# Kernel optimization log

Measured on AMD Instinct MI355X. Metric: run time of the kernel, lower is better.

The kernel has to match this reference:

```python
import jax, jax.numpy as jnp
import numpy as np

N, D, K_FRAC = 4096, 256, 0.5
EPS = 1e-5  # BatchNorm1d default eps


def setup_inputs() -> dict:
    key = jax.random.key(0)
    kg, kh, kw = jax.random.split(key, 3)
    # sparse binary adjacency with self-loops so all degrees > 0 (pow(D,-1) finite)
    g = (jax.random.uniform(kg, (N, N)) < 0.004).astype(jnp.float32)
    g = jnp.maximum(g, jnp.eye(N, dtype=jnp.float32))
    h = jax.random.normal(kh, (N, D), dtype=jnp.float32)
    return {
        "g": g,
        "h": h,
        "gamma": jnp.ones((D,), jnp.float32),
        "beta": jnp.zeros((D,), jnp.float32),
        "w_proj": jax.random.normal(kw, (D, 1), dtype=jnp.float32) / np.sqrt(D),
        "b_proj": jnp.zeros((1,), jnp.float32),
        "sigma1": jnp.array([0.2], jnp.float32),
    }


def reference(g, h, gamma, beta, w_proj, b_proj, sigma1):
    # BatchNorm1d in training mode: batch statistics over the node axis
    mu = h.mean(0)
    var = h.var(0)  # biased variance, as torch uses for normalization
    h = (h - mu) / jnp.sqrt(var + EPS) * gamma + beta

    deg = g.sum(1)                               # [N] == Z2
    agg = (g @ h) / deg[:, None]                 # diag(D^-1) @ (g @ h), no NxN diag materialized
    Z1 = jnp.abs(h - agg).sum(1)                 # [N]
    pl = jax.nn.sigmoid(Z1 + deg)
    Z3 = (agg @ w_proj + b_proj)[:, 0]           # proj(Z3).squeeze()
    pg = jax.nn.softmax(Z3)                      # 1-D softmax (dim 0)
    pt = jax.nn.sigmoid(pl + pg)
    pf = jax.nn.sigmoid((h @ w_proj + b_proj)[:, 0])
    scores = sigma1[0] * pt + (1.0 - sigma1[0]) * pf

    # top_k_graph
    k = max(2, int(K_FRAC * N))
    _, idx = jax.lax.top_k(scores, k)            # [k]
    h_att = scores[:, None] * h                  # score-weighted features
    un_g = (g != 0).astype(jnp.float32)
    two_hop = ((un_g @ un_g) != 0).astype(jnp.float32)  # binarized 2-hop adjacency
    a_hat = two_hop[idx, :]                      # [k, N] row gather
    new_h = a_hat @ h_att                        # [k, D]
    g_new = a_hat[:, idx]                        # [k, k] column gather
    # norm_g: torch broadcast divides COLUMN j by row-sum degrees[j]
    g_new = g_new / g_new.sum(1)
    return g_new, new_h, idx
```

## Files before the change

### kernel.cpp

```cpp
#include <hip/hip_runtime.h>
#include <math.h>

#define NN 4096
#define DD 256
#define KK 2048
#define NW 64
#define SK 4
#define KC (NN / SK)
#define KW (KC / 32)

typedef float f32x4  __attribute__((ext_vector_type(4)));
typedef short bf16x8 __attribute__((ext_vector_type(8)));

__device__ __forceinline__ int build_list(const unsigned long long* __restrict__ B, int r,
                                          int l, int* cols, int cap) {
    unsigned long long word = B[(size_t)r * NW + l];
    int pc = __popcll(word);
    int off = pc;
    for (int d = 1; d < 64; d <<= 1) {
        int n = __shfl_up(off, d);
        if (l >= d) off += n;
    }
    int total = __shfl(off, 63);
    int base = off - pc;
    while (word) {
        int b = (int)__ffsll(word) - 1;
        word &= word - 1;
        if (base < cap) cols[base] = l * 64 + b;
        ++base;
    }
    return total;
}

__global__ void k_pre(const float* __restrict__ h, const float* __restrict__ g,
                      double* __restrict__ psum, double* __restrict__ psq,
                      unsigned long long* __restrict__ B) {
    int blk = blockIdx.x;
    int t = threadIdx.x;
    if (blk < 64) {
        int d = t;
        int r0 = blk * 64;
        double s0=0,s1=0,s2=0,s3=0,q0=0,q1=0,q2=0,q3=0;
        for (int k = 0; k < 64; k += 4) {
            double x0 = (double)h[(size_t)(r0+k+0) * DD + d];
            double x1 = (double)h[(size_t)(r0+k+1) * DD + d];
            double x2 = (double)h[(size_t)(r0+k+2) * DD + d];
            double x3 = (double)h[(size_t)(r0+k+3) * DD + d];
            s0 += x0; q0 += x0*x0;
            s1 += x1; q1 += x1*x1;
            s2 += x2; q2 += x2*x2;
            s3 += x3; q3 += x3*x3;
        }
        psum[blk * DD + d] = (s0+s1)+(s2+s3);
        psq [blk * DD + d] = (q0+q1)+(q2+q3);
    } else {
        int i = blk - 64;
        int q = t >> 6, l = t & 63;
        const float* gr = g + (size_t)i * NN;
        unsigned long long word = 0ull;
        int lw = l & 15;
        #pragma unroll
        for (int wi = 0; wi < 16; ++wi) {
            float v = gr[(q * 16 + wi) * 64 + l];
            unsigned long long m = __ballot(v != 0.0f);
            if (wi == lw) word = m;
        }
        if (l < 16) B[(size_t)i * NW + q * 16 + l] = word;
    }
}

__global__ void k_stats_final(const double* __restrict__ psum, const double* __restrict__ psq,
                              double* __restrict__ mu, double* __restrict__ rstd) {
    __shared__ double rs[4][DD];
    __shared__ double rq[4][DD];
    int t = threadIdx.x;
    int d = t & (DD - 1);
    int q = t >> 8;
    double s0=0,s1=0,q0=0,q1=0;
    int b0 = q * 16;
    for (int k = 0; k < 16; k += 2) {
        s0 += psum[(b0+k)   * DD + d];
        s1 += psum[(b0+k+1) * DD + d];
        q0 += psq [(b0+k)   * DD + d];
        q1 += psq [(b0+k+1) * DD + d];
    }
    rs[q][d] = s0 + s1;
    rq[q][d] = q0 + q1;
    __syncthreads();
    if (q == 0) {
        double S  = (rs[0][d]+rs[1][d]) + (rs[2][d]+rs[3][d]);
        double Q  = (rq[0][d]+rq[1][d]) + (rq[2][d]+rq[3][d]);
        double m  = S / (double)NN;
        double var = Q / (double)NN - m * m;
        mu[d]   = m;
        rstd[d] = 1.0 / sqrt(var + 1e-5);
    }
}

__global__ void k_main(const float* __restrict__ h, const double* __restrict__ mu,
                       const double* __restrict__ rstd, const float* __restrict__ gamma,
                       const float* __restrict__ beta, const unsigned long long* __restrict__ Bm,
                       const float* __restrict__ w, const float* __restrict__ bp,
                       float* __restrict__ hn, double* __restrict__ zpf,
                       unsigned long long* __restrict__ T, double* __restrict__ Z1,
                       double* __restrict__ Z3, int* __restrict__ degi) {
    __shared__ int cols[4][136];
    int blk = blockIdx.x;
    int t = threadIdx.x;
    int wv = t >> 6, l = t & 63;
    int r = blk * 4 + wv;
    int cnt = build_list(Bm, r, l, cols[wv], 128);
    if (cnt > 128) cnt = 128;
    const float4* h4 = (const float4*)h;
    double s0=0,s1=0,s2=0,s3=0,u0=0,u1=0,u2=0,u3=0;
    unsigned long long a0 = 0ull, a1 = 0ull;
    int j = 0;
    for (; j + 1 < cnt; j += 2) {
        int c0 = cols[wv][j], c1 = cols[wv][j + 1];
        float4 v0 = h4[(size_t)c0 * 64 + l];
        float4 v1 = h4[(size_t)c1 * 64 + l];
        a0 |= Bm[(size_t)c0 * NW + l];
        a1 |= Bm[(size_t)c1 * NW + l];
        s0 += (double)v0.x; s1 += (double)v0.y; s2 += (double)v0.z; s3 += (double)v0.w;
        u0 += (double)v1.x; u1 += (double)v1.y; u2 += (double)v1.z; u3 += (double)v1.w;
    }
    if (j < cnt) {
        int c0 = cols[wv][j];
        float4 v0 = h4[(size_t)c0 * 64 + l];
        a0 |= Bm[(size_t)c0 * NW + l];
        s0 += (double)v0.x; s1 += (double)v0.y; s2 += (double)v0.z; s3 += (double)v0.w;
    }
    T[(size_t)r * NW + l] = a0 | a1;
    s0 += u0; s1 += u1; s2 += u2; s3 += u3;
    const double2* mu2 = (const double2*)mu;
    const double2* rs2 = (const double2*)rstd;
    const float4*  ga4 = (const float4*)gamma;
    const float4*  be4 = (const float4*)beta;
    const float4*  w4  = (const float4*)w;
    double2 mA = mu2[2*l], mB = mu2[2*l+1];
    double2 rA = rs2[2*l], rB = rs2[2*l+1];
    float4 ga = ga4[l], be = be4[l], wl = w4[l];
    double inv = 1.0 / (double)cnt;
    double g0 = (s0 * inv - mA.x) * rA.x * (double)ga.x + (double)be.x;
    double g1 = (s1 * inv - mA.y) * rA.y * (double)ga.y + (double)be.y;
    double g2 = (s2 * inv - mB.x) * rB.x * (double)ga.z + (double)be.z;
    double g3 = (s3 * inv - mB.y) * rB.y * (double)ga.w + (double)be.w;
    float4 hv = h4[(size_t)r * 64 + l];
    double h0 = ((double)hv.x - mA.x) * rA.x * (double)ga.x + (double)be.x;
    double h1 = ((double)hv.y - mA.y) * rA.y * (double)ga.y + (double)be.y;
    double h2 = ((double)hv.z - mB.x) * rB.x * (double)ga.z + (double)be.z;
    double h3 = ((double)hv.w - mB.y) * rB.y * (double)ga.w + (double)be.w;
    float4 o = { (float)h0, (float)h1, (float)h2, (float)h3 };
    ((float4*)hn)[(size_t)r * 64 + l] = o;
    double z1p = (fabs(h0 - g0) + fabs(h1 - g1)) + (fabs(h2 - g2) + fabs(h3 - g3));
    double z3p = (g0 * (double)wl.x + g1 * (double)wl.y)
               + (g2 * (double)wl.z + g3 * (double)wl.w);
    double zfp = (h0 * (double)wl.x + h1 * (double)wl.y)
               + (h2 * (double)wl.z + h3 * (double)wl.w);
    for (int off = 32; off > 0; off >>= 1) {
        z1p += __shfl_down(z1p, off);
        z3p += __shfl_down(z3p, off);
        zfp += __shfl_down(zfp, off);
    }
    if (l == 0) {
        Z1[r] = z1p;
        Z3[r] = z3p + (double)bp[0];
        zpf[r] = zfp + (double)bp[0];
        degi[r] = cnt;
    }
}

__global__ void k_sel(const double* __restrict__ Z1, const double* __restrict__ Z3,
                      const double* __restrict__ zpf, const int* __restrict__ degi,
                      const float* __restrict__ sigma1, const float* __restrict__ hn,
                      unsigned short* __restrict__ haT_hi, unsigned short* __restrict__ haT_lo,
                      int* __restrict__ idx_int, float* __restrict__ out_idx) {
    __shared__ unsigned long long Kl[NN];
    double* red = (double*)Kl;
    int bid = blockIdx.x;
    int t = threadIdx.x;
    int wv = t >> 6, l = t & 63;
    double mx = -1e300;
    for (int k = 0; k < 16; ++k) mx = fmax(mx, Z3[t + 256 * k]);
    red[t] = mx;
    __syncthreads();
    for (int s = 128; s > 0; s >>= 1) {
        if (t < s) red[t] = fmax(red[t], red[t + s]);
        __syncthreads();
    }
    double M = red[0];
    __syncthreads();
    double se = 0.0;
    for (int k = 0; k < 16; ++k) se += exp(Z3[t + 256 * k] - M);
    red[t] = se;
    __syncthreads();
    for (int s = 128; s > 0; s >>= 1) {
        if (t < s) red[t] += red[t + s];
        __syncthreads();
    }
    double sum = red[0];
    double s1 = (double)sigma1[0];
    __syncthreads();
    if (bid < 256) {
        for (int i = t; i < NN; i += 256) {
            double pg = exp(Z3[i] - M) / sum;
            double pl = 1.0 / (1.0 + exp(-(Z1[i] + (double)degi[i])));
            double pt = 1.0 / (1.0 + exp(-(pl + pg)));
            double pf = 1.0 / (1.0 + exp(-zpf[i]));
            float sc = (float)(s1 * pt + (1.0 - s1) * pf);
            unsigned int b2 = __float_as_uint(sc);
            unsigned int ka = (b2 & 0x80000000u) ? ~b2 : (b2 ^ 0x80000000u);
            Kl[i] = ((unsigned long long)(~ka) << 32) | (unsigned int)i;
        }
        __syncthreads();
        int il = t >> 4, sub = t & 15;
        int i = bid * 16 + il;
        unsigned long long ki = Kl[i];
        int c0 = 0, c1 = 0, c2 = 0, c3 = 0;
        for (int jj = 0; jj < 256; jj += 4) {
            int jx = sub + (jj << 4);
            c0 += (Kl[jx]      < ki) ? 1 : 0;
            c1 += (Kl[jx + 16] < ki) ? 1 : 0;
            c2 += (Kl[jx + 32] < ki) ? 1 : 0;
            c3 += (Kl[jx + 48] < ki) ? 1 : 0;
        }
        int cnt = (c0 + c1) + (c2 + c3);
        for (int off = 8; off > 0; off >>= 1) cnt += __shfl_down(cnt, off, 16);
        if (sub == 0 && cnt < KK) {
            idx_int[cnt] = i;
            out_idx[cnt] = (float)i;
        }
    } else {
        int bb = bid - 256;
        int ng = bb & 63, dq = bb >> 6;
        int node = ng * 64 + l;
        double pg = exp(Z3[node] - M) / sum;
        double pl = 1.0 / (1.0 + exp(-(Z1[node] + (double)degi[node])));
        double pt = 1.0 / (1.0 + exp(-(pl + pg)));
        double pf = 1.0 / (1.0 + exp(-zpf[node]));
        float sc = (float)(s1 * pt + (1.0 - s1) * pf);
        const float* hr = hn + (size_t)node * DD;
        for (int d = dq * 64 + wv; d < (dq + 1) * 64; d += 4) {
            float x = hr[d] * sc;
            unsigned int xb = __float_as_uint(x);
            unsigned int hb = xb & 0xFFFF0000u;
            float lo = x - __uint_as_float(hb);
            unsigned int lb = __float_as_uint(lo);
            haT_hi[(size_t)d * NN + node] = (unsigned short)(hb >> 16);
            haT_lo[(size_t)d * NN + node] = (unsigned short)(lb >> 16);
        }
    }
}

__global__ void k_out(const unsigned long long* __restrict__ T, const int* __restrict__ idx_int,
                      const unsigned short* __restrict__ haT_hi,
                      const unsigned short* __restrict__ haT_lo,
                      float* __restrict__ part, float* __restrict__ out_gnew) {
    union Sm {
        struct { unsigned long long Tl[NW]; int redc[4]; } og;
        struct { int ids[128]; unsigned int Ab[128][KW + 1]; } nh;
    };
    __shared__ Sm sm;
    int bid = blockIdx.x;
    int t = threadIdx.x;
    int wv = t >> 6, l = t & 63;
    if (bid < 256) {
        int blk = bid;
        int rs = blk & 15, cb = (blk >> 4) & 3, kc = blk >> 6;
        if (t < 128) sm.nh.ids[t] = idx_int[rs * 128 + t];
        __syncthreads();
        for (int i = t; i < 128 * KW; i += 256) {
            int row = i >> 5, wd = i & (KW - 1);
            sm.nh.Ab[row][wd] =
                ((const unsigned int*)(T + (size_t)sm.nh.ids[row] * NW))[kc * KW + wd];
        }
        __syncthreads();
        int lm = l & 15, lg = l >> 4;
        int row_base = (wv & 1) * 64;
        int col_base = cb * 64 + (wv >> 1) * 32;
        f32x4 acc[4][2];
        #pragma unroll
        for (int m = 0; m < 4; ++m) { acc[m][0] = (f32x4)0.0f; acc[m][1] = (f32x4)0.0f; }
        const unsigned short* ph0 = haT_hi + (size_t)(col_base + lm) * NN + kc * KC + lg * 8;
        const unsigned short* ph1 = ph0 + (size_t)16 * NN;
        const unsigned short* pl0 = haT_lo + (size_t)(col_base + lm) * NN + kc * KC + lg * 8;
        const unsigned short* pl1 = pl0 + (size_t)16 * NN;
        #pragma unroll 2
        for (int ks = 0; ks < KW; ++ks) {
            bf16x8 bh0 = *(const bf16x8*)(ph0 + ks * 32);
            bf16x8 bh1 = *(const bf16x8*)(ph1 + ks * 32);
            bf16x8 bl0 = *(const bf16x8*)(pl0 + ks * 32);
            bf16x8 bl1 = *(const bf16x8*)(pl1 + ks * 32);
            #pragma unroll
            for (int m = 0; m < 4; ++m) {
                unsigned int bits = sm.nh.Ab[row_base + m * 16 + lm][ks];
                unsigned int b8 = (bits >> (8 * lg)) & 0xFFu;
                union { unsigned int u[4]; bf16x8 v; } au;
                au.u[0] = ((b8 & 1u)        ? 0x3F80u : 0u) | ((b8 & 2u)   ? 0x3F800000u : 0u);
                au.u[1] = (((b8 >> 2) & 1u) ? 0x3F80u : 0u) | ((b8 & 8u)   ? 0x3F800000u : 0u);
                au.u[2] = (((b8 >> 4) & 1u) ? 0x3F80u : 0u) | ((b8 & 32u)  ? 0x3F800000u : 0u);
                au.u[3] = (((b8 >> 6) & 1u) ? 0x3F80u : 0u) | ((b8 & 128u) ? 0x3F800000u : 0u);
                bf16x8 a = au.v;
                acc[m][0] = __builtin_amdgcn_mfma_f32_16x16x32_bf16(a, bh0, acc[m][0], 0, 0, 0);
                acc[m][1] = __builtin_amdgcn_mfma_f32_16x16x32_bf16(a, bh1, acc[m][1], 0, 0, 0);
                acc[m][0] = __builtin_amdgcn_mfma_f32_16x16x32_bf16(a, bl0, acc[m][0], 0, 0, 0);
                acc[m][1] = __builtin_amdgcn_mfma_f32_16x16x32_bf16(a, bl1, acc[m][1], 0, 0, 0);
            }
        }
        float* pp = part + (size_t)kc * ((size_t)KK * DD);
        #pragma unroll
        for (int m = 0; m < 4; ++m) {
            int row0 = rs * 128 + row_base + m * 16 + lg * 4;
            #pragma unroll
            for (int n = 0; n < 2; ++n) {
                int col = col_base + n * 16 + lm;
                #pragma unroll
                for (int rr = 0; rr < 4; ++rr)
                    pp[(size_t)(row0 + rr) * DD + col] = acc[m][n][rr];
            }
        }
    } else {
        int r = bid - 256;
        if (t < NW) sm.og.Tl[t] = T[(size_t)idx_int[r] * NW + t];
        __syncthreads();
        const int4* idx4 = (const int4*)idx_int;
        int cloc = 0;
        for (int c4 = t; c4 < KK / 4; c4 += 256) {
            int4 jc = idx4[c4];
            cloc += (int)((sm.og.Tl[jc.x >> 6] >> (jc.x & 63)) & 1ull)
                  + (int)((sm.og.Tl[jc.y >> 6] >> (jc.y & 63)) & 1ull)
                  + (int)((sm.og.Tl[jc.z >> 6] >> (jc.z & 63)) & 1ull)
                  + (int)((sm.og.Tl[jc.w >> 6] >> (jc.w & 63)) & 1ull);
        }
        for (int off = 32; off > 0; off >>= 1) cloc += __shfl_down(cloc, off);
        if (l == 0) sm.og.redc[wv] = cloc;
        __syncthreads();
        float inv = 1.0f / (float)((sm.og.redc[0] + sm.og.redc[1])
                                 + (sm.og.redc[2] + sm.og.redc[3]));
        float4* out4 = (float4*)(out_gnew + (size_t)r * KK);
        for (int c4 = t; c4 < KK / 4; c4 += 256) {
            int4 jc = idx4[c4];
            float4 o;
            o.x = ((sm.og.Tl[jc.x >> 6] >> (jc.x & 63)) & 1ull) ? inv : 0.0f;
            o.y = ((sm.og.Tl[jc.y >> 6] >> (jc.y & 63)) & 1ull) ? inv : 0.0f;
            o.z = ((sm.og.Tl[jc.z >> 6] >> (jc.z & 63)) & 1ull) ? inv : 0.0f;
            o.w = ((sm.og.Tl[jc.w >> 6] >> (jc.w & 63)) & 1ull) ? inv : 0.0f;
            out4[c4] = o;
        }
    }
}

__global__ void k_red(const float* __restrict__ part, float* __restrict__ out_newh) {
    int t = threadIdx.x;
    size_t off = (size_t)blockIdx.x * 1024 + (size_t)t * 4;
    const size_t stride = (size_t)KK * DD;
    float4 s0 = *(const float4*)(part + off);
    float4 s1 = *(const float4*)(part + off + stride);
    float4 s2 = *(const float4*)(part + off + 2 * stride);
    float4 s3 = *(const float4*)(part + off + 3 * stride);
    float4 o;
    o.x = (s0.x + s1.x) + (s2.x + s3.x);
    o.y = (s0.y + s1.y) + (s2.y + s3.y);
    o.z = (s0.z + s1.z) + (s2.z + s3.z);
    o.w = (s0.w + s1.w) + (s2.w + s3.w);
    *(float4*)(out_newh + off) = o;
}

extern "C" void kernel_launch(void* const* d_in, const int* in_sizes, int n_in,
                              void* d_out, int out_size, void* d_ws, size_t ws_size,
                              hipStream_t stream) {
    const float* g      = (const float*)d_in[0];
    const float* h      = (const float*)d_in[1];
    const float* gamma  = (const float*)d_in[2];
    const float* beta   = (const float*)d_in[3];
    const float* w_proj = (const float*)d_in[4];
    const float* b_proj = (const float*)d_in[5];
    const float* sigma1 = (const float*)d_in[6];

    char* p = (char*)d_ws;
    auto alloc = [&](size_t bytes) -> void* {
        void* q = (void*)p;
        p += (bytes + 255) & ~(size_t)255;
        return q;
    };
    double* psum    = (double*)alloc(64 * DD * 8);
    double* psq     = (double*)alloc(64 * DD * 8);
    double* mu      = (double*)alloc(DD * 8);
    double* rstd    = (double*)alloc(DD * 8);
    double* zpf     = (double*)alloc(NN * 8);
    double* Z1      = (double*)alloc(NN * 8);
    double* Z3      = (double*)alloc(NN * 8);
    int*    degi    = (int*)alloc(NN * 4);
    int*    idx_int = (int*)alloc(KK * 4);
    unsigned long long* B = (unsigned long long*)alloc((size_t)NN * NW * 8);
    unsigned long long* T = (unsigned long long*)alloc((size_t)NN * NW * 8);
    float*  hn      = (float*)alloc((size_t)NN * DD * 4);
    unsigned short* haT_hi = (unsigned short*)alloc((size_t)DD * NN * 2);
    unsigned short* haT_lo = (unsigned short*)alloc((size_t)DD * NN * 2);
    float*  part    = (float*)alloc((size_t)SK * KK * DD * 4);

    float* out_gnew = (float*)d_out;
    float* out_newh = out_gnew + (size_t)KK * KK;
    float* out_idx  = out_newh + (size_t)KK * DD;

    hipLaunchKernelGGL(k_pre,         dim3(64 + NN), dim3(256),  0, stream, h, g, psum, psq, B);
    hipLaunchKernelGGL(k_stats_final, dim3(1),       dim3(1024), 0, stream, psum, psq, mu, rstd);
    hipLaunchKernelGGL(k_main,        dim3(NN / 4),  dim3(256),  0, stream, h, mu, rstd, gamma, beta, B, w_proj, b_proj, hn, zpf, T, Z1, Z3, degi);
    hipLaunchKernelGGL(k_sel,         dim3(512),     dim3(256),  0, stream, Z1, Z3, zpf, degi, sigma1, hn, haT_hi, haT_lo, idx_int, out_idx);
    hipLaunchKernelGGL(k_out,         dim3(256 + KK), dim3(256), 0, stream, T, idx_int, haT_hi, haT_lo, part, out_gnew);
    hipLaunchKernelGGL(k_red,         dim3(512),     dim3(256),  0, stream, part, out_newh);
}
```

Baseline: 179.2 us.

## Hoist score/key computation into own kernel and drop split-K reduction for new_h

Score and sort-key computation, previously repeated redundantly in each of the 512 selection blocks (softmax max/sum plus per-node exps), now runs once in a small 16-block kernel that writes scores and keys to global memory. The selection kernel then only loads the keys and scores. The new_h matmul no longer splits K four ways into a partial buffer followed by a separate reduction kernel. Each block now loops over all K chunks with a smaller 128x16 output tile and writes the result directly, which removes the partial-buffer traffic and one launch. The cost is an extra launch and less register reuse per MFMA tile, with more serial K work per block.

After: 188.3 us. 1.05x slower.

```diff
diff --git a/kernel.cpp b/kernel.cpp
--- a/kernel.cpp
+++ b/kernel.cpp
@@ -170,16 +170,12 @@
     }
 }
 
-__global__ void k_sel(const double* __restrict__ Z1, const double* __restrict__ Z3,
-                      const double* __restrict__ zpf, const int* __restrict__ degi,
-                      const float* __restrict__ sigma1, const float* __restrict__ hn,
-                      unsigned short* __restrict__ haT_hi, unsigned short* __restrict__ haT_lo,
-                      int* __restrict__ idx_int, float* __restrict__ out_idx) {
-    __shared__ unsigned long long Kl[NN];
-    double* red = (double*)Kl;
-    int bid = blockIdx.x;
-    int t = threadIdx.x;
-    int wv = t >> 6, l = t & 63;
+__global__ void k_scorekeys(const double* __restrict__ Z1, const double* __restrict__ Z3,
+                            const double* __restrict__ zpf, const int* __restrict__ degi,
+                            const float* __restrict__ sigma1, float* __restrict__ scores,
+                            unsigned long long* __restrict__ keys) {
+    __shared__ double red[256];
+    int t = threadIdx.x;
     double mx = -1e300;
     for (int k = 0; k < 16; ++k) mx = fmax(mx, Z3[t + 256 * k]);
     red[t] = mx;
@@ -199,19 +195,29 @@
         __syncthreads();
     }
     double sum = red[0];
+    int i = blockIdx.x * 256 + t;
     double s1 = (double)sigma1[0];
-    __syncthreads();
+    double pg = exp(Z3[i] - M) / sum;
+    double pl = 1.0 / (1.0 + exp(-(Z1[i] + (double)degi[i])));
+    double pt = 1.0 / (1.0 + exp(-(pl + pg)));
+    double pf = 1.0 / (1.0 + exp(-zpf[i]));
+    float sc = (float)(s1 * pt + (1.0 - s1) * pf);
+    scores[i] = sc;
+    unsigned int b2 = __float_as_uint(sc);
+    unsigned int ka = (b2 & 0x80000000u) ? ~b2 : (b2 ^ 0x80000000u);
+    keys[i] = ((unsigned long long)(~ka) << 32) | (unsigned int)i;
+}
+
+__global__ void k_sel(const unsigned long long* __restrict__ keys,
+                      const float* __restrict__ scores, const float* __restrict__ hn,
+                      unsigned short* __restrict__ haT_hi, unsigned short* __restrict__ haT_lo,
+                      int* __restrict__ idx_int, float* __restrict__ out_idx) {
+    __shared__ unsigned long long Kl[NN];
+    int bid = blockIdx.x;
+    int t = threadIdx.x;
+    int wv = t >> 6, l = t & 63;
     if (bid < 256) {
-        for (int i = t; i < NN; i += 256) {
-            double pg = exp(Z3[i] - M) / sum;
-            double pl = 1.0 / (1.0 + exp(-(Z1[i] + (double)degi[i])));
-            double pt = 1.0 / (1.0 + exp(-(pl + pg)));
-            double pf = 1.0 / (1.0 + exp(-zpf[i]));
-            float sc = (float)(s1 * pt + (1.0 - s1) * pf);
-            unsigned int b2 = __float_as_uint(sc);
-            unsigned int ka = (b2 & 0x80000000u) ? ~b2 : (b2 ^ 0x80000000u);
-            Kl[i] = ((unsigned long long)(~ka) << 32) | (unsigned int)i;
-        }
+        for (int i = t; i < NN; i += 256) Kl[i] = keys[i];
         __syncthreads();
         int il = t >> 4, sub = t & 15;
         int i = bid * 16 + il;
@@ -234,11 +240,7 @@
         int bb = bid - 256;
         int ng = bb & 63, dq = bb >> 6;
         int node = ng * 64 + l;
-        double pg = exp(Z3[node] - M) / sum;
-        double pl = 1.0 / (1.0 + exp(-(Z1[node] + (double)degi[node])));
-        double pt = 1.0 / (1.0 + exp(-(pl + pg)));
-        double pf = 1.0 / (1.0 + exp(-zpf[node]));
-        float sc = (float)(s1 * pt + (1.0 - s1) * pf);
+        float sc = scores[node];
         const float* hr = hn + (size_t)node * DD;
         for (int d = dq * 64 + wv; d < (dq + 1) * 64; d += 4) {
             float x = hr[d] * sc;
@@ -255,7 +257,7 @@
 __global__ void k_out(const unsigned long long* __restrict__ T, const int* __restrict__ idx_int,
                       const unsigned short* __restrict__ haT_hi,
                       const unsigned short* __restrict__ haT_lo,
-                      float* __restrict__ part, float* __restrict__ out_gnew) {
+                      float* __restrict__ out_gnew, float* __restrict__ out_newh) {
     union Sm {
         struct { unsigned long long Tl[NW]; int redc[4]; } og;
         struct { int ids[128]; unsigned int Ab[128][KW + 1]; } nh;
@@ -265,60 +267,55 @@
     int t = threadIdx.x;
     int wv = t >> 6, l = t & 63;
     if (bid < 256) {
-        int blk = bid;
-        int rs = blk & 15, cb = (blk >> 4) & 3, kc = blk >> 6;
+        int rs = bid >> 4, cb = bid & 15;
         if (t < 128) sm.nh.ids[t] = idx_int[rs * 128 + t];
-        __syncthreads();
-        for (int i = t; i < 128 * KW; i += 256) {
-            int row = i >> 5, wd = i & (KW - 1);
-            sm.nh.Ab[row][wd] =
-                ((const unsigned int*)(T + (size_t)sm.nh.ids[row] * NW))[kc * KW + wd];
-        }
-        __syncthreads();
         int lm = l & 15, lg = l >> 4;
-        int row_base = (wv & 1) * 64;
-        int col_base = cb * 64 + (wv >> 1) * 32;
-        f32x4 acc[4][2];
+        int row_base = wv * 32;
+        int col_base = cb * 16;
+        f32x4 acc0 = (f32x4)0.0f, acc1 = (f32x4)0.0f;
+        const unsigned short* ph = haT_hi + (size_t)(col_base + lm) * NN + lg * 8;
+        const unsigned short* pl = haT_lo + (size_t)(col_base + lm) * NN + lg * 8;
+        for (int kc = 0; kc < SK; ++kc) {
+            __syncthreads();
+            for (int i = t; i < 128 * KW; i += 256) {
+                int row = i >> 5, wd = i & (KW - 1);
+                sm.nh.Ab[row][wd] =
+                    ((const unsigned int*)(T + (size_t)sm.nh.ids[row] * NW))[kc * KW + wd];
+            }
+            __syncthreads();
+            const unsigned short* phk = ph + kc * KC;
+            const unsigned short* plk = pl + kc * KC;
+            #pragma unroll 4
+            for (int ks = 0; ks < KW; ++ks) {
+                bf16x8 bh = *(const bf16x8*)(phk + ks * 32);
+                bf16x8 bl = *(const bf16x8*)(plk + ks * 32);
+                unsigned int bits0 = sm.nh.Ab[row_base + lm][ks];
+                unsigned int bits1 = sm.nh.Ab[row_base + 16 + lm][ks];
+                unsigned int b80 = (bits0 >> (8 * lg)) & 0xFFu;
+                unsigned int b81 = (bits1 >> (8 * lg)) & 0xFFu;
+                union { unsigned int u[4]; bf16x8 v; } a0, a1;
+                a0.u[0] = ((b80 & 1u)        ? 0x3F80u : 0u) | ((b80 & 2u)   ? 0x3F800000u : 0u);
+                a0.u[1] = (((b80 >> 2) & 1u) ? 0x3F80u : 0u) | ((b80 & 8u)   ? 0x3F800000u : 0u);
+                a0.u[2] = (((b80 >> 4) & 1u) ? 0x3F80u : 0u) | ((b80 & 32u)  ? 0x3F800000u : 0u);
+                a0.u[3] = (((b80 >> 6) & 1u) ? 0x3F80u : 0u) | ((b80 & 128u) ? 0x3F800000u : 0u);
+                a1.u[0] = ((b81 & 1u)        ? 0x3F80u : 0u) | ((b81 & 2u)   ? 0x3F800000u : 0u);
+                a1.u[1] = (((b81 >> 2) & 1u) ? 0x3F80u : 0u) | ((b81 & 8u)   ? 0x3F800000u : 0u);
+                a1.u[2] = (((b81 >> 4) & 1u) ? 0x3F80u : 0u) | ((b81 & 32u)  ? 0x3F800000u : 0u);
+                a1.u[3] = (((b81 >> 6) & 1u) ? 0x3F80u : 0u) | ((b81 & 128u) ? 0x3F800000u : 0u);
+                acc0 = __builtin_amdgcn_mfma_f32_16x16x32_bf16(a0.v, bh, acc0, 0, 0, 0);
+                acc1 = __builtin_amdgcn_mfma_f32_16x16x32_bf16(a1.v, bh, acc1, 0, 0, 0);
+                acc0 = __builtin_amdgcn_mfma_f32_16x16x32_bf16(a0.v, bl, acc0, 0, 0, 0);
+                acc1 = __builtin_amdgcn_mfma_f32_16x16x32_bf16(a1.v, bl, acc1, 0, 0, 0);
+            }
+        }
+        int col = col_base + lm;
+        int row0 = rs * 128 + row_base + lg * 4;
         #pragma unroll
-        for (int m = 0; m < 4; ++m) { acc[m][0] = (f32x4)0.0f; acc[m][1] = (f32x4)0.0f; }
-        const unsigned short* ph0 = haT_hi + (size_t)(col_base + lm) * NN + kc * KC + lg * 8;
-        const unsigned short* ph1 = ph0 + (size_t)16 * NN;
-        const unsigned short* pl0 = haT_lo + (size_t)(col_base + lm) * NN + kc * KC + lg * 8;
-        const unsigned short* pl1 = pl0 + (size_t)16 * NN;
-        #pragma unroll 2
-        for (int ks = 0; ks < KW; ++ks) {
-            bf16x8 bh0 = *(const bf16x8*)(ph0 + ks * 32);
-            bf16x8 bh1 = *(const bf16x8*)(ph1 + ks * 32);
-            bf16x8 bl0 = *(const bf16x8*)(pl0 + ks * 32);
-            bf16x8 bl1 = *(const bf16x8*)(pl1 + ks * 32);
-            #pragma unroll
-            for (int m = 0; m < 4; ++m) {
-                unsigned int bits = sm.nh.Ab[row_base + m * 16 + lm][ks];
-                unsigned int b8 = (bits >> (8 * lg)) & 0xFFu;
-                union { unsigned int u[4]; bf16x8 v; } au;
-                au.u[0] = ((b8 & 1u)        ? 0x3F80u : 0u) | ((b8 & 2u)   ? 0x3F800000u : 0u);
-                au.u[1] = (((b8 >> 2) & 1u) ? 0x3F80u : 0u) | ((b8 & 8u)   ? 0x3F800000u : 0u);
-                au.u[2] = (((b8 >> 4) & 1u) ? 0x3F80u : 0u) | ((b8 & 32u)  ? 0x3F800000u : 0u);
-                au.u[3] = (((b8 >> 6) & 1u) ? 0x3F80u : 0u) | ((b8 & 128u) ? 0x3F800000u : 0u);
-                bf16x8 a = au.v;
-                acc[m][0] = __builtin_amdgcn_mfma_f32_16x16x32_bf16(a, bh0, acc[m][0], 0, 0, 0);
-                acc[m][1] = __builtin_amdgcn_mfma_f32_16x16x32_bf16(a, bh1, acc[m][1], 0, 0, 0);
-                acc[m][0] = __builtin_amdgcn_mfma_f32_16x16x32_bf16(a, bl0, acc[m][0], 0, 0, 0);
-                acc[m][1] = __builtin_amdgcn_mfma_f32_16x16x32_bf16(a, bl1, acc[m][1], 0, 0, 0);
-            }
-        }
-        float* pp = part + (size_t)kc * ((size_t)KK * DD);
+        for (int rr = 0; rr < 4; ++rr)
+            out_newh[(size_t)(row0 + rr) * DD + col] = acc0[rr];
         #pragma unroll
-        for (int m = 0; m < 4; ++m) {
-            int row0 = rs * 128 + row_base + m * 16 + lg * 4;
-            #pragma unroll
-            for (int n = 0; n < 2; ++n) {
-                int col = col_base + n * 16 + lm;
-                #pragma unroll
-                for (int rr = 0; rr < 4; ++rr)
-                    pp[(size_t)(row0 + rr) * DD + col] = acc[m][n][rr];
-            }
-        }
+        for (int rr = 0; rr < 4; ++rr)
+            out_newh[(size_t)(row0 + 16 + rr) * DD + col] = acc1[rr];
     } else {
         int r = bid - 256;
         if (t < NW) sm.og.Tl[t] = T[(size_t)idx_int[r] * NW + t];
@@ -348,22 +345,6 @@
             out4[c4] = o;
         }
     }
-}
-
-__global__ void k_red(const float* __restrict__ part, float* __restrict__ out_newh) {
-    int t = threadIdx.x;
-    size_t off = (size_t)blockIdx.x * 1024 + (size_t)t * 4;
-    const size_t stride = (size_t)KK * DD;
-    float4 s0 = *(const float4*)(part + off);
-    float4 s1 = *(const float4*)(part + off + stride);
-    float4 s2 = *(const float4*)(part + off + 2 * stride);
-    float4 s3 = *(const float4*)(part + off + 3 * stride);
-    float4 o;
-    o.x = (s0.x + s1.x) + (s2.x + s3.x);
-    o.y = (s0.y + s1.y) + (s2.y + s3.y);
-    o.z = (s0.z + s1.z) + (s2.z + s3.z);
-    o.w = (s0.w + s1.w) + (s2.w + s3.w);
-    *(float4*)(out_newh + off) = o;
 }
 
 extern "C" void kernel_launch(void* const* d_in, const int* in_sizes, int n_in,
@@ -391,22 +372,23 @@
     double* Z1      = (double*)alloc(NN * 8);
     double* Z3      = (double*)alloc(NN * 8);
     int*    degi    = (int*)alloc(NN * 4);
+    float*  scores  = (float*)alloc(NN * 4);
+    unsigned long long* keys = (unsigned long long*)alloc(NN * 8);
     int*    idx_int = (int*)alloc(KK * 4);
     unsigned long long* B = (unsigned long long*)alloc((size_t)NN * NW * 8);
     unsigned long long* T = (unsigned long long*)alloc((size_t)NN * NW * 8);
     float*  hn      = (float*)alloc((size_t)NN * DD * 4);
     unsigned short* haT_hi = (unsigned short*)alloc((size_t)DD * NN * 2);
     unsigned short* haT_lo = (unsigned short*)alloc((size_t)DD * NN * 2);
-    float*  part    = (float*)alloc((size_t)SK * KK * DD * 4);
 
     float* out_gnew = (float*)d_out;
     float* out_newh = out_gnew + (size_t)KK * KK;
     float* out_idx  = out_newh + (size_t)KK * DD;
 
-    hipLaunchKernelGGL(k_pre,         dim3(64 + NN), dim3(256),  0, stream, h, g, psum, psq, B);
-    hipLaunchKernelGGL(k_stats_final, dim3(1),       dim3(1024), 0, stream, psum, psq, mu, rstd);
-    hipLaunchKernelGGL(k_main,        dim3(NN / 4),  dim3(256),  0, stream, h, mu, rstd, gamma, beta, B, w_proj, b_proj, hn, zpf, T, Z1, Z3, degi);
-    hipLaunchKernelGGL(k_sel,         dim3(512),     dim3(256),  0, stream, Z1, Z3, zpf, degi, sigma1, hn, haT_hi, haT_lo, idx_int, out_idx);
-    hipLaunchKernelGGL(k_out,         dim3(256 + KK), dim3(256), 0, stream, T, idx_int, haT_hi, haT_lo, part, out_gnew);
-    hipLaunchKernelGGL(k_red,         dim3(512),     dim3(256),  0, stream, part, out_newh);
-}
+    hipLaunchKernelGGL(k_pre,         dim3(64 + NN),  dim3(256),  0, stream, h, g, psum, psq, B);
+    hipLaunchKernelGGL(k_stats_final, dim3(1),        dim3(1024), 0, stream, psum, psq, mu, rstd);
+    hipLaunchKernelGGL(k_main,        dim3(NN / 4),   dim3(256),  0, stream, h, mu, rstd, gamma, beta, B, w_proj, b_proj, hn, zpf, T, Z1, Z3, degi);
+    hipLaunchKernelGGL(k_scorekeys,   dim3(16),       dim3(256),  0, stream, Z1, Z3, zpf, degi, sigma1, scores, keys);
+    hipLaunchKernelGGL(k_sel,         dim3(512),      dim3(256),  0, stream, keys, scores, hn, haT_hi, haT_lo, idx_int, out_idx);
+    hipLaunchKernelGGL(k_out,         dim3(256 + KK), dim3(256),  0, stream, T, idx_int, haT_hi, haT_lo, out_gnew, out_newh);
+}
```
